# Kernel optimization log

Measured on AMD Instinct MI355X. Metric: run time of the kernel, lower is better.

The kernel has to match this reference:

```python
import jax, jax.numpy as jnp
import numpy as np

NUM_BLOCKS = 8
BLOCK_SIZE = 96  # hidden_size 768 / 8
HSF = 1          # hidden_size_factor
LAM = 0.01       # sparsity_threshold
HARD_FRAC = 1.0
SCALE = 0.02


def setup_inputs() -> dict:
    key = jax.random.key(0)
    k = jax.random.split(key, 5)
    x = jax.random.normal(k[0], (1, 768, 256, 512), dtype=jnp.float32)
    w1 = SCALE * jax.random.normal(k[1], (NUM_BLOCKS, BLOCK_SIZE, BLOCK_SIZE * HSF, 2), dtype=jnp.float32)
    b1 = SCALE * jax.random.normal(k[2], (NUM_BLOCKS, BLOCK_SIZE * HSF, 1, 1, 2), dtype=jnp.float32)
    w2 = SCALE * jax.random.normal(k[3], (NUM_BLOCKS, BLOCK_SIZE * HSF, BLOCK_SIZE, 2), dtype=jnp.float32)
    b2 = SCALE * jax.random.normal(k[4], (NUM_BLOCKS, BLOCK_SIZE, 1, 1, 2), dtype=jnp.float32)
    return {"x": x, "w1": w1, "b1": b1, "w2": w2, "b2": b2}


def _cplx(t):
    # last-dim [re, im] real layout -> complex
    return jax.lax.complex(t[..., 0], t[..., 1])


def _softshrink(v, lam):
    return jnp.sign(v) * jnp.maximum(jnp.abs(v) - lam, 0.0)


def reference(x, w1, b1, w2, b2):
    B, C, H, W = x.shape
    bias = x
    Wc = W // 2 + 1
    total_modes = H // 2 + 1
    kept_modes = int(total_modes * HARD_FRAC)
    hs = total_modes - kept_modes
    he = min(total_modes + kept_modes, H)  # torch slicing clamps

    # rfft2 over (H, W), ortho norm; split channels into blocks
    xf = jnp.fft.rfft2(x.astype(jnp.float32), s=(H, W), axes=(-2, -1), norm="ortho")
    xf = xf.reshape(B, NUM_BLOCKS, BLOCK_SIZE, H, Wc)

    a = xf[:, :, :, hs:he, :kept_modes]  # kept modes only
    w1c, b1c = _cplx(w1), _cplx(b1)
    w2c, b2c = _cplx(w2), _cplx(b2)

    # block-diagonal complex matmul + bias; ReLU applied to re/im independently
    t1 = jnp.einsum("bkixy,kio->bkoxy", a, w1c) + b1c
    o1 = jax.lax.complex(jax.nn.relu(t1.real), jax.nn.relu(t1.imag))
    t2 = jnp.einsum("bkixy,kio->bkoxy", o1, w2c) + b2c
    # softshrink per real/imag component (softshrink(0)=0, so zero-padded modes stay zero)
    s = jax.lax.complex(_softshrink(t2.real, LAM), _softshrink(t2.imag, LAM))

    o2 = jnp.zeros((B, NUM_BLOCKS, BLOCK_SIZE, H, Wc), dtype=s.dtype)
    o2 = o2.at[:, :, :, hs:he, :kept_modes].set(s)

    out = jnp.fft.irfft2(o2.reshape(B, C, H, Wc), s=(H, W), axes=(-2, -1), norm="ortho")
    return out.astype(x.dtype) + bias
```

## Files before the change

### kernel.cpp

```cpp
#include <hip/hip_runtime.h>
#include <math.h>

#define HH 256
#define WW 512
#define CC 768
#define KW 129
#define NB 8
#define BS 96
#define MPC (KW*HH)
#define K3M 64

constexpr float SF = 0.00276213586400528f;
constexpr float SI = 0.00552427172801056f;
constexpr float LAM = 0.01f;

#define SWZ(i) ((i) ^ (((i) >> 4) & 0xF))
#define TSWZ(i) ((i) ^ ((((i) >> 4) & 7) << 1) ^ (((i) >> 7) & 1))

__device__ inline float2 cadd(float2 a, float2 b) { return make_float2(a.x + b.x, a.y + b.y); }
__device__ inline float2 csub(float2 a, float2 b) { return make_float2(a.x - b.x, a.y - b.y); }
__device__ inline float2 cmul(float2 a, float2 b) {
    return make_float2(a.x * b.x - a.y * b.y, a.x * b.y + a.y * b.x);
}

__device__ inline void gen_tw(float2* tw, int tid, int nthr, float sign) {
    for (int f = tid; f < 255; f += nthr) {
        int fm = f, n = 256;
        while (fm >= (n >> 1)) { fm -= (n >> 1); n >>= 1; }
        float sn, cs;
        __sincosf(sign * 6.283185307179586f * (float)fm / (float)n, &sn, &cs);
        tw[f] = make_float2(cs, sn);
    }
}

__device__ inline void fft256x4(float2* s0, float2* s1, const float2* tw, int lane) {
    float2* src = s0;
    float2* dst = s1;
    int logls = 0;
    int offA = 0;
#pragma unroll
    for (int j = 0; j < 4; j++) {
        int ls = 1 << logls;
        int hm = 64 >> logls;
        int offB = offA + (128 >> logls);
        int q = lane & (ls - 1);
        int p = lane >> logls;
        float2 a0 = src[SWZ(lane)];
        float2 a1 = src[SWZ(lane + 64)];
        float2 a2 = src[SWZ(lane + 128)];
        float2 a3 = src[SWZ(lane + 192)];
        float2 wA0 = tw[offA + p];
        float2 wA1 = tw[offA + p + hm];
        float2 wB  = tw[offB + p];
        float2 e0 = cadd(a0, a2);
        float2 e1 = cmul(csub(a0, a2), wA0);
        float2 e2 = cadd(a1, a3);
        float2 e3 = cmul(csub(a1, a3), wA1);
        float2 f0 = cadd(e0, e2);
        float2 f1 = cmul(csub(e0, e2), wB);
        float2 f2 = cadd(e1, e3);
        float2 f3 = cmul(csub(e1, e3), wB);
        int o = q + ((p << logls) << 2);
        dst[SWZ(o)]          = f0;
        dst[SWZ(o + ls)]     = f2;
        dst[SWZ(o + 2 * ls)] = f1;
        dst[SWZ(o + 3 * ls)] = f3;
        __syncthreads();
        float2* tmp = src; src = dst; dst = tmp;
        offA = offB + hm;
        logls += 2;
    }
}

__global__ __launch_bounds__(512) void k1_rfftw(const float* __restrict__ x,
                                                float2* __restrict__ A) {
    __shared__ float2 b0[8][256];
    __shared__ float2 b1[8][256];
    __shared__ float2 tile[KW * 8];
    __shared__ float2 tw[255];
    __shared__ float2 ctw[129];

    int tid = threadIdx.x;
    gen_tw(tw, tid, 512, -1.0f);
    for (int f = tid; f < 129; f += 512) {
        float sn, cs;
        __sincosf(-6.283185307179586f * (float)f / 512.0f, &sn, &cs);
        ctw[f] = make_float2(cs, sn);
    }

    int r = tid >> 6;
    int lane = tid & 63;
    int blk = blockIdx.x;
    int c = blk >> 5;
    int h0 = (blk & 31) << 3;
    int h = h0 + r;

    const float4* xrow = (const float4*)(x + ((size_t)c * HH + h) * WW);
    float2* s0 = b0[r];
    float2* s1 = b1[r];

    for (int n = lane; n < 128; n += 64) {
        float4 v = xrow[n];
        s0[SWZ(2 * n)]     = make_float2(v.x * SF, v.y * SF);
        s0[SWZ(2 * n + 1)] = make_float2(v.z * SF, v.w * SF);
    }
    __syncthreads();

    fft256x4(s0, s1, tw, lane);

    for (int k = lane; k <= 128; k += 64) {
        float2 Za = s0[SWZ(k & 255)];
        float2 Zb = s0[SWZ((256 - k) & 255)];
        float2 Xe = make_float2(0.5f * (Za.x + Zb.x), 0.5f * (Za.y - Zb.y));
        float dx = Za.x - Zb.x;
        float dy = Za.y + Zb.y;
        float2 Xo = make_float2(0.5f * dy, -0.5f * dx);
        float2 X = cadd(Xe, cmul(Xo, ctw[k]));
        tile[TSWZ(k * 8 + r)] = X;
    }
    __syncthreads();

    for (int idx = tid; idx < KW * 8; idx += 512) {
        int k = idx >> 3;
        int r2 = idx & 7;
        A[((size_t)c * KW + k) * HH + h0 + r2] = tile[TSWZ(idx)];
    }
}

template <int SIGN>
__global__ __launch_bounds__(256) void k_colfft(float2* __restrict__ A) {
    __shared__ float2 b0[4][256];
    __shared__ float2 b1[4][256];
    __shared__ float2 tw[255];
    int tid = threadIdx.x;
    gen_tw(tw, tid, 256, (float)SIGN);
    int col = tid >> 6;
    int lane = tid & 63;
    size_t base = ((size_t)blockIdx.x * 4 + col) * 256;
    float2* s0 = b0[col];
    float2* s1 = b1[col];
    const float4* Ai = (const float4*)(A + base);
    for (int n = lane; n < 128; n += 64) {
        float4 v = Ai[n];
        s0[SWZ(2 * n)]     = make_float2(v.x, v.y);
        s0[SWZ(2 * n + 1)] = make_float2(v.z, v.w);
    }
    __syncthreads();
    fft256x4(s0, s1, tw, lane);
    float4* Ao = (float4*)(A + base);
    for (int n = lane; n < 128; n += 64) {
        float2 z0 = s0[SWZ(2 * n)];
        float2 z1 = s0[SWZ(2 * n + 1)];
        Ao[n] = make_float4(z0.x, z0.y, z1.x, z1.y);
    }
}

__global__ __launch_bounds__(512, 4) void k3_mlp(float2* __restrict__ A,
                                                 const float2* __restrict__ w1,
                                                 const float2* __restrict__ b1,
                                                 const float2* __restrict__ w2,
                                                 const float2* __restrict__ b2) {
    __shared__ float2 tile[BS][K3M];
    __shared__ float2 wt[BS][32];
    int tid = threadIdx.x;
    int bk = blockIdx.x / (MPC / K3M);
    int m0 = (blockIdx.x % (MPC / K3M)) * K3M;
    int t = tid & 63;
    int osu = __builtin_amdgcn_readfirstlane(tid >> 6);
    int ob = osu * 4;

    for (int idx = tid; idx < BS * (K3M / 2); idx += 512) {
        int i = idx >> 5;
        int tt = idx & 31;
        float4 v = *(const float4*)(A + ((size_t)(bk * BS + i)) * MPC + m0 + 2 * tt);
        tile[i][2 * tt]     = make_float2(v.x, v.y);
        tile[i][2 * tt + 1] = make_float2(v.z, v.w);
    }

    const float2* w1b = w1 + (size_t)bk * BS * BS;
    const float2* b1b = b1 + (size_t)bk * BS;
    const float2* w2b = w2 + (size_t)bk * BS * BS;
    const float2* b2b = b2 + (size_t)bk * BS;

    float2 hreg[12];
#pragma unroll
    for (int ph = 0; ph < 3; ph++) {
        int o0 = ph * 32;
        __syncthreads();
        for (int idx = tid; idx < BS * 32; idx += 512) {
            int i = idx >> 5;
            int j = idx & 31;
            wt[i][j] = w1b[i * BS + o0 + j];
        }
        __syncthreads();
        float2 acc0 = b1b[o0 + ob];
        float2 acc1 = b1b[o0 + ob + 1];
        float2 acc2 = b1b[o0 + ob + 2];
        float2 acc3 = b1b[o0 + ob + 3];
#pragma unroll 8
        for (int i = 0; i < BS; i++) {
            float2 a  = tile[i][t];
            float4 w01 = *(const float4*)&wt[i][ob];
            float4 w23 = *(const float4*)&wt[i][ob + 2];
            acc0.x = fmaf(a.x, w01.x, fmaf(-a.y, w01.y, acc0.x));
            acc0.y = fmaf(a.x, w01.y, fmaf(a.y, w01.x, acc0.y));
            acc1.x = fmaf(a.x, w01.z, fmaf(-a.y, w01.w, acc1.x));
            acc1.y = fmaf(a.x, w01.w, fmaf(a.y, w01.z, acc1.y));
            acc2.x = fmaf(a.x, w23.x, fmaf(-a.y, w23.y, acc2.x));
            acc2.y = fmaf(a.x, w23.y, fmaf(a.y, w23.x, acc2.y));
            acc3.x = fmaf(a.x, w23.z, fmaf(-a.y, w23.w, acc3.x));
            acc3.y = fmaf(a.x, w23.w, fmaf(a.y, w23.z, acc3.y));
        }
        hreg[ph * 4 + 0] = make_float2(fmaxf(acc0.x, 0.f), fmaxf(acc0.y, 0.f));
        hreg[ph * 4 + 1] = make_float2(fmaxf(acc1.x, 0.f), fmaxf(acc1.y, 0.f));
        hreg[ph * 4 + 2] = make_float2(fmaxf(acc2.x, 0.f), fmaxf(acc2.y, 0.f));
        hreg[ph * 4 + 3] = make_float2(fmaxf(acc3.x, 0.f), fmaxf(acc3.y, 0.f));
    }
    __syncthreads();
#pragma unroll
    for (int ph = 0; ph < 3; ph++) {
        int o = ph * 32 + ob;
        tile[o][t]     = hreg[ph * 4 + 0];
        tile[o + 1][t] = hreg[ph * 4 + 1];
        tile[o + 2][t] = hreg[ph * 4 + 2];
        tile[o + 3][t] = hreg[ph * 4 + 3];
    }

#pragma unroll
    for (int ph = 0; ph < 3; ph++) {
        int o0 = ph * 32;
        __syncthreads();
        for (int idx = tid; idx < BS * 32; idx += 512) {
            int i = idx >> 5;
            int j = idx & 31;
            wt[i][j] = w2b[i * BS + o0 + j];
        }
        __syncthreads();
        float2 acc0 = b2b[o0 + ob];
        float2 acc1 = b2b[o0 + ob + 1];
        float2 acc2 = b2b[o0 + ob + 2];
        float2 acc3 = b2b[o0 + ob + 3];
#pragma unroll 8
        for (int i = 0; i < BS; i++) {
            float2 a  = tile[i][t];
            float4 w01 = *(const float4*)&wt[i][ob];
            float4 w23 = *(const float4*)&wt[i][ob + 2];
            acc0.x = fmaf(a.x, w01.x, fmaf(-a.y, w01.y, acc0.x));
            acc0.y = fmaf(a.x, w01.y, fmaf(a.y, w01.x, acc0.y));
            acc1.x = fmaf(a.x, w01.z, fmaf(-a.y, w01.w, acc1.x));
            acc1.y = fmaf(a.x, w01.w, fmaf(a.y, w01.z, acc1.y));
            acc2.x = fmaf(a.x, w23.x, fmaf(-a.y, w23.y, acc2.x));
            acc2.y = fmaf(a.x, w23.y, fmaf(a.y, w23.x, acc2.y));
            acc3.x = fmaf(a.x, w23.z, fmaf(-a.y, w23.w, acc3.x));
            acc3.y = fmaf(a.x, w23.w, fmaf(a.y, w23.z, acc3.y));
        }
        float2 accs[4] = {acc0, acc1, acc2, acc3};
#pragma unroll
        for (int j = 0; j < 4; j++) {
            float rx = fmaxf(fabsf(accs[j].x) - LAM, 0.f);
            float ry = fmaxf(fabsf(accs[j].y) - LAM, 0.f);
            float2 sv = make_float2(copysignf(rx, accs[j].x), copysignf(ry, accs[j].y));
            A[((size_t)(bk * BS + o0 + ob + j)) * MPC + m0 + t] = sv;
        }
    }
}

__global__ __launch_bounds__(512) void k5_irfftw(const float2* __restrict__ A,
                                                 const float* __restrict__ x,
                                                 float* __restrict__ out) {
    __shared__ float2 b0[8][256];
    __shared__ float2 b1[8][256];
    __shared__ float2 tile[KW * 8];
    __shared__ float2 tw[255];
    __shared__ float2 ctw[256];

    int tid = threadIdx.x;
    gen_tw(tw, tid, 512, 1.0f);
    for (int f = tid; f < 256; f += 512) {
        float sn, cs;
        __sincosf(6.283185307179586f * (float)f / 512.0f, &sn, &cs);
        ctw[f] = make_float2(cs, sn);
    }

    int blk = blockIdx.x;
    int c = blk >> 5;
    int h0 = (blk & 31) << 3;

    for (int idx = tid; idx < KW * 8; idx += 512) {
        int k = idx >> 3;
        int r2 = idx & 7;
        tile[TSWZ(idx)] = A[((size_t)c * KW + k) * HH + h0 + r2];
    }
    __syncthreads();

    int r = tid >> 6;
    int lane = tid & 63;
    int h = h0 + r;
    float2* s0 = b0[r];
    float2* s1 = b1[r];

    for (int k = lane; k < 256; k += 64) {
        float2 P = make_float2(0.f, 0.f);
        float2 Q = make_float2(0.f, 0.f);
        if (k <= 128) {
            P = tile[TSWZ(k * 8 + r)];
            if (k == 0) P.y = 0.f;
        }
        if (k >= 128) {
            float2 qv = tile[TSWZ((256 - k) * 8 + r)];
            Q = make_float2(qv.x, -qv.y);
        }
        float2 Xe = make_float2(0.5f * (P.x + Q.x), 0.5f * (P.y + Q.y));
        float2 d = make_float2(0.5f * (P.x - Q.x), 0.5f * (P.y - Q.y));
        float2 Xo = cmul(d, ctw[k]);
        s0[SWZ(k)] = make_float2(Xe.x - Xo.y, Xe.y + Xo.x);
    }
    __syncthreads();

    fft256x4(s0, s1, tw, lane);

    const float4* xr = (const float4*)(x + ((size_t)c * HH + h) * WW);
    float4* orow = (float4*)(out + ((size_t)c * HH + h) * WW);
    for (int m = lane; m < 128; m += 64) {
        float2 z0 = s0[SWZ(2 * m)];
        float2 z1 = s0[SWZ(2 * m + 1)];
        float4 xv = xr[m];
        orow[m] = make_float4(fmaf(SI, z0.x, xv.x), fmaf(SI, z0.y, xv.y),
                              fmaf(SI, z1.x, xv.z), fmaf(SI, z1.y, xv.w));
    }
}

extern "C" void kernel_launch(void* const* d_in, const int* in_sizes, int n_in,
                              void* d_out, int out_size, void* d_ws, size_t ws_size,
                              hipStream_t stream) {
    const float* x = (const float*)d_in[0];
    const float2* w1 = (const float2*)d_in[1];
    const float2* b1 = (const float2*)d_in[2];
    const float2* w2 = (const float2*)d_in[3];
    const float2* b2 = (const float2*)d_in[4];
    float* out = (float*)d_out;
    float2* A = (float2*)d_ws;

    k1_rfftw<<<dim3(CC * HH / 8), dim3(512), 0, stream>>>(x, A);
    k_colfft<-1><<<dim3(CC * KW / 4), dim3(256), 0, stream>>>(A);
    k3_mlp<<<dim3(NB * (MPC / K3M)), dim3(512), 0, stream>>>(A, w1, b1, w2, b2);
    k_colfft<1><<<dim3(CC * KW / 4), dim3(256), 0, stream>>>(A);
    k5_irfftw<<<dim3(CC * HH / 8), dim3(512), 0, stream>>>(A, x, out);
}
```

Measured before the change: 1.524 ms.

## Replace block barriers in FFT with wave-level LDS waits; read MLP weights directly

Inside the 256-point FFT and before it in the inverse kernel, the block-wide __syncthreads is replaced by a per-wave LDS wait (s_waitcnt lgkmcnt(0) between scheduling barriers). This relies on each row's FFT being handled entirely by one 64-lane wave, so cross-wave barriers should be unnecessary. The MLP kernel drops the shared weight-staging buffer and its barriers and loads weights straight from global memory as wave-uniform float4 reads, with fewer syncs overall. The tile fill also becomes a single float4 LDS store. The risks are races if any FFT stage actually depends on data from other waves, and weaker weight reuse because each wave now fetches weights from cache instead of shared memory.

```diff
diff --git a/kernel.cpp b/kernel.cpp
--- a/kernel.cpp
+++ b/kernel.cpp
@@ -21,6 +21,12 @@
 __device__ inline float2 csub(float2 a, float2 b) { return make_float2(a.x - b.x, a.y - b.y); }
 __device__ inline float2 cmul(float2 a, float2 b) {
     return make_float2(a.x * b.x - a.y * b.y, a.x * b.y + a.y * b.x);
+}
+
+__device__ inline void wsync() {
+    __builtin_amdgcn_sched_barrier(0);
+    asm volatile("s_waitcnt lgkmcnt(0)" ::: "memory");
+    __builtin_amdgcn_sched_barrier(0);
 }
 
 __device__ inline void gen_tw(float2* tw, int tid, int nthr, float sign) {
@@ -65,7 +71,7 @@
         dst[SWZ(o + ls)]     = f2;
         dst[SWZ(o + 2 * ls)] = f1;
         dst[SWZ(o + 3 * ls)] = f3;
-        __syncthreads();
+        wsync();
         float2* tmp = src; src = dst; dst = tmp;
         offA = offB + hm;
         logls += 2;
@@ -161,20 +167,18 @@
                                                  const float2* __restrict__ w2,
                                                  const float2* __restrict__ b2) {
     __shared__ float2 tile[BS][K3M];
-    __shared__ float2 wt[BS][32];
     int tid = threadIdx.x;
     int bk = blockIdx.x / (MPC / K3M);
     int m0 = (blockIdx.x % (MPC / K3M)) * K3M;
     int t = tid & 63;
-    int osu = __builtin_amdgcn_readfirstlane(tid >> 6);
+    int osu = tid >> 6;
     int ob = osu * 4;
 
     for (int idx = tid; idx < BS * (K3M / 2); idx += 512) {
         int i = idx >> 5;
         int tt = idx & 31;
         float4 v = *(const float4*)(A + ((size_t)(bk * BS + i)) * MPC + m0 + 2 * tt);
-        tile[i][2 * tt]     = make_float2(v.x, v.y);
-        tile[i][2 * tt + 1] = make_float2(v.z, v.w);
+        *(float4*)&tile[i][2 * tt] = v;
     }
 
     const float2* w1b = w1 + (size_t)bk * BS * BS;
@@ -182,26 +186,22 @@
     const float2* w2b = w2 + (size_t)bk * BS * BS;
     const float2* b2b = b2 + (size_t)bk * BS;
 
+    __syncthreads();
+
     float2 hreg[12];
 #pragma unroll
     for (int ph = 0; ph < 3; ph++) {
-        int o0 = ph * 32;
-        __syncthreads();
-        for (int idx = tid; idx < BS * 32; idx += 512) {
-            int i = idx >> 5;
-            int j = idx & 31;
-            wt[i][j] = w1b[i * BS + o0 + j];
-        }
-        __syncthreads();
-        float2 acc0 = b1b[o0 + ob];
-        float2 acc1 = b1b[o0 + ob + 1];
-        float2 acc2 = b1b[o0 + ob + 2];
-        float2 acc3 = b1b[o0 + ob + 3];
-#pragma unroll 8
+        int o0 = ph * 32 + ob;
+        const float2* wp = w1b + o0;
+        float2 acc0 = b1b[o0];
+        float2 acc1 = b1b[o0 + 1];
+        float2 acc2 = b1b[o0 + 2];
+        float2 acc3 = b1b[o0 + 3];
+#pragma unroll 4
         for (int i = 0; i < BS; i++) {
             float2 a  = tile[i][t];
-            float4 w01 = *(const float4*)&wt[i][ob];
-            float4 w23 = *(const float4*)&wt[i][ob + 2];
+            float4 w01 = *(const float4*)(wp + (size_t)i * BS);
+            float4 w23 = *(const float4*)(wp + (size_t)i * BS + 2);
             acc0.x = fmaf(a.x, w01.x, fmaf(-a.y, w01.y, acc0.x));
             acc0.y = fmaf(a.x, w01.y, fmaf(a.y, w01.x, acc0.y));
             acc1.x = fmaf(a.x, w01.z, fmaf(-a.y, w01.w, acc1.x));
@@ -225,26 +225,21 @@
         tile[o + 2][t] = hreg[ph * 4 + 2];
         tile[o + 3][t] = hreg[ph * 4 + 3];
     }
+    __syncthreads();
 
 #pragma unroll
     for (int ph = 0; ph < 3; ph++) {
-        int o0 = ph * 32;
-        __syncthreads();
-        for (int idx = tid; idx < BS * 32; idx += 512) {
-            int i = idx >> 5;
-            int j = idx & 31;
-            wt[i][j] = w2b[i * BS + o0 + j];
-        }
-        __syncthreads();
-        float2 acc0 = b2b[o0 + ob];
-        float2 acc1 = b2b[o0 + ob + 1];
-        float2 acc2 = b2b[o0 + ob + 2];
-        float2 acc3 = b2b[o0 + ob + 3];
-#pragma unroll 8
+        int o0 = ph * 32 + ob;
+        const float2* wp = w2b + o0;
+        float2 acc0 = b2b[o0];
+        float2 acc1 = b2b[o0 + 1];
+        float2 acc2 = b2b[o0 + 2];
+        float2 acc3 = b2b[o0 + 3];
+#pragma unroll 4
         for (int i = 0; i < BS; i++) {
             float2 a  = tile[i][t];
-            float4 w01 = *(const float4*)&wt[i][ob];
-            float4 w23 = *(const float4*)&wt[i][ob + 2];
+            float4 w01 = *(const float4*)(wp + (size_t)i * BS);
+            float4 w23 = *(const float4*)(wp + (size_t)i * BS + 2);
             acc0.x = fmaf(a.x, w01.x, fmaf(-a.y, w01.y, acc0.x));
             acc0.y = fmaf(a.x, w01.y, fmaf(a.y, w01.x, acc0.y));
             acc1.x = fmaf(a.x, w01.z, fmaf(-a.y, w01.w, acc1.x));
@@ -260,7 +255,7 @@
             float rx = fmaxf(fabsf(accs[j].x) - LAM, 0.f);
             float ry = fmaxf(fabsf(accs[j].y) - LAM, 0.f);
             float2 sv = make_float2(copysignf(rx, accs[j].x), copysignf(ry, accs[j].y));
-            A[((size_t)(bk * BS + o0 + ob + j)) * MPC + m0 + t] = sv;
+            A[((size_t)(bk * BS + o0 + j)) * MPC + m0 + t] = sv;
         }
     }
 }
@@ -315,7 +310,7 @@
         float2 Xo = cmul(d, ctw[k]);
         s0[SWZ(k)] = make_float2(Xe.x - Xo.y, Xe.y + Xo.x);
     }
-    __syncthreads();
+    wsync();
 
     fft256x4(s0, s1, tw, lane);
 
```

Result: slower. 2.095 ms (+37.5%).
